# Performance work log

Hardware: AMD Instinct MI355X
Metric: run time of the kernel (lower is better)

Reference implementation:

```python
import jax, jax.numpy as jnp
import numpy as np

B, T, N, E = 4, 16, 1024, 16384
F_IN, H, FF, NH, L, C = 128, 256, 1024, 8, 2, 10
HD = H // NH
EPS = 1e-5


def setup_inputs() -> dict:
    key = jax.random.key(0)
    ks = jax.random.split(key, 12)
    g = lambda k, s: jax.random.normal(k, s, dtype=jnp.float32) * 0.02
    return {
        "x": jax.random.normal(ks[0], (B, T, N, F_IN), dtype=jnp.float32),
        "edge_index": jax.random.randint(ks[1], (B, T, 2, E), 0, N, dtype=jnp.int32),
        # GraphSAGE layer 1 (PyG SAGEConv: lin_l on mean-aggregated neighbors, lin_r on self)
        "sage1_Wl": g(ks[2], (F_IN, H)), "sage1_bl": jnp.zeros((H,), jnp.float32),
        "sage1_Wr": g(ks[3], (F_IN, H)),
        # GraphSAGE layer 2
        "sage2_Wl": g(ks[4], (H, H)), "sage2_bl": jnp.zeros((H,), jnp.float32),
        "sage2_Wr": g(ks[5], (H, H)),
        # TransformerEncoder, stacked over L layers
        "Wqkv": g(ks[6], (L, H, 3 * H)), "bqkv": jnp.zeros((L, 3 * H), jnp.float32),
        "Wo": g(ks[7], (L, H, H)), "bo": jnp.zeros((L, H), jnp.float32),
        "ln1_s": jnp.ones((L, H), jnp.float32), "ln1_b": jnp.zeros((L, H), jnp.float32),
        "W1": g(ks[8], (L, H, FF)), "b1": jnp.zeros((L, FF), jnp.float32),
        "W2": g(ks[9], (L, FF, H)), "b2": jnp.zeros((L, H), jnp.float32),
        "ln2_s": jnp.ones((L, H), jnp.float32), "ln2_b": jnp.zeros((L, H), jnp.float32),
        # final classifier
        "fc_W": g(ks[10], (H, C)), "fc_b": jnp.zeros((C,), jnp.float32),
    }


def _sage_conv(x, src, dst, Wl, bl, Wr):
    # mean neighbor aggregation: for each target node, mean of source features
    deg = jax.ops.segment_sum(jnp.ones((E,), x.dtype), dst, num_segments=N)
    agg = jax.ops.segment_sum(x[src], dst, num_segments=N)  # [N, F]
    agg = agg / jnp.clip(deg, 1.0)[:, None]
    return agg @ Wl + bl + x @ Wr


def _layernorm(x, s, b):
    m = jnp.mean(x, axis=-1, keepdims=True)
    v = jnp.var(x, axis=-1, keepdims=True)
    return (x - m) * jax.lax.rsqrt(v + EPS) * s + b


def _encoder_layer(h, Wqkv, bqkv, Wo, bo, ln1_s, ln1_b, W1, b1, W2, b2, ln2_s, ln2_b):
    # h: [B, T, H] -- post-norm (PyTorch default norm_first=False), relu FFN
    qkv = h @ Wqkv + bqkv  # [B, T, 3H]
    q, k, v = jnp.split(qkv, 3, axis=-1)
    sp = lambda t: t.reshape(B, T, NH, HD).transpose(0, 2, 1, 3)  # [B, NH, T, HD]
    q, k, v = sp(q), sp(k), sp(v)
    scores = jnp.einsum("bhqd,bhkd->bhqk", q, k) / np.sqrt(HD).astype(np.float32)
    attn = jax.nn.softmax(scores, axis=-1)
    ctx = jnp.einsum("bhqk,bhkd->bhqd", attn, v)
    ctx = ctx.transpose(0, 2, 1, 3).reshape(B, T, H)
    h = _layernorm(h + ctx @ Wo + bo, ln1_s, ln1_b)
    ffn = jax.nn.relu(h @ W1 + b1) @ W2 + b2
    return _layernorm(h + ffn, ln2_s, ln2_b)


def reference(x, edge_index, sage1_Wl, sage1_bl, sage1_Wr, sage2_Wl, sage2_bl,
              sage2_Wr, Wqkv, bqkv, Wo, bo, ln1_s, ln1_b, W1, b1, W2, b2,
              ln2_s, ln2_b, fc_W, fc_b):
    xf = x.reshape(B * T, N, F_IN)
    ef = edge_index.reshape(B * T, 2, E)

    def per_graph(xg, eg):
        src, dst = eg[0], eg[1]
        h = jax.nn.relu(_sage_conv(xg, src, dst, sage1_Wl, sage1_bl, sage1_Wr))
        h = _sage_conv(h, src, dst, sage2_Wl, sage2_bl, sage2_Wr)
        return jnp.mean(h, axis=0)  # mean-pool over nodes -> [H]

    emb = jax.vmap(per_graph)(xf, ef).reshape(B, T, H)

    h = emb
    for l in range(L):
        h = _encoder_layer(h, Wqkv[l], bqkv[l], Wo[l], bo[l], ln1_s[l], ln1_b[l],
                           W1[l], b1[l], W2[l], b2[l], ln2_s[l], ln2_b[l])
    return h[:, -1, :] @ fc_W + fc_b  # [B, C]
```

## Files before the change

kernel.cpp:

```cpp
#include <hip/hip_runtime.h>
#include <hip/hip_bf16.h>

#define Bc 4
#define Tc 16
#define Nc 1024
#define Ec 16384
#define FIN 128
#define Hc 256
#define FFc 1024
#define NHc 8
#define Lc 2
#define HDc 32
#define Gc 64
#define EPSc 1e-5f

typedef __bf16 v8bf __attribute__((ext_vector_type(8)));
typedef float v4f __attribute__((ext_vector_type(4)));

__global__ __launch_bounds__(1024) void prep_kernel(
        const int* __restrict__ ei, const float* __restrict__ Wl, const float* __restrict__ Wr,
        float* __restrict__ invdeg, float* __restrict__ cw, int* __restrict__ off,
        unsigned short* __restrict__ elist, float* __restrict__ uv,
        __bf16* __restrict__ pH, __bf16* __restrict__ pL) {
    __shared__ int degs[Nc];
    __shared__ float inv[Nc];
    __shared__ float cl[Nc];
    __shared__ int wsum[16];
    if (blockIdx.x >= 64) {
        int id = (blockIdx.x - 64) * 1024 + threadIdx.x;
        int t = id & 511;
        int bidOld = id >> 9;
        int lane = t >> 3, j = t & 7;
        int kc = bidOld >> 4, nt = bidOld & 15;
        int k = kc * 32 + ((lane >> 4) << 3) + j;
        int n = nt * 16 + (lane & 15);
        float wv = (k < 128) ? Wl[(size_t)k * Hc + n] : Wr[(size_t)(k - 128) * Hc + n];
        __bf16 hi = (__bf16)wv;
        pH[id] = hi;
        pL[id] = (__bf16)(wv - (float)hi);
        return;
    }
    int g = blockIdx.x, t = threadIdx.x;
    const int* src = ei + (size_t)g * 2 * Ec;
    const int* dst = src + Ec;
    if (t < 512) uv[g * 512 + t] = 0.f;
    degs[t] = 0; cl[t] = 0.f;
    __syncthreads();
    for (int e = t; e < Ec; e += 1024) atomicAdd(&degs[dst[e] & (Nc - 1)], 1);
    __syncthreads();
    float iv = 1.0f / fmaxf((float)degs[t], 1.0f);
    inv[t] = iv;
    invdeg[g * Nc + t] = iv;
    __syncthreads();
    for (int e = t; e < Ec; e += 1024) atomicAdd(&cl[src[e] & (Nc - 1)], inv[dst[e] & (Nc - 1)]);
    __syncthreads();
    cw[g * Nc + t] = cl[t];
    int own = degs[t];
    int lane = t & 63, wv2 = t >> 6;
    int val = own;
#pragma unroll
    for (int ofs = 1; ofs < 64; ofs <<= 1) {
        int v = __shfl_up(val, ofs, 64);
        if (lane >= ofs) val += v;
    }
    if (lane == 63) wsum[wv2] = val;
    __syncthreads();
    if (wv2 == 0 && lane < 16) {
        int wval = wsum[lane];
#pragma unroll
        for (int ofs = 1; ofs < 16; ofs <<= 1) {
            int v = __shfl_up(wval, ofs, 64);
            if (lane >= ofs) wval += v;
        }
        wsum[lane] = wval;
    }
    __syncthreads();
    int incl = val + ((wv2 > 0) ? wsum[wv2 - 1] : 0);
    int excl = incl - own;
    off[g * 1032 + t] = excl;
    if (t == 1023) off[g * 1032 + Nc] = incl;
    degs[t] = excl;
    __syncthreads();
    for (int e = t; e < Ec; e += 1024) {
        int d = dst[e] & (Nc - 1);
        int slot = atomicAdd(&degs[d], 1);
        elist[(size_t)g * Ec + slot] = (unsigned short)(src[e] & (Nc - 1));
    }
}

__global__ __launch_bounds__(512, 4) void sage_kernel(
        const float* __restrict__ x, const unsigned short* __restrict__ elist,
        const int* __restrict__ off, const float* __restrict__ invdeg,
        const float* __restrict__ cw, const __bf16* __restrict__ pH,
        const __bf16* __restrict__ pL, const float* __restrict__ bias,
        float* __restrict__ uv) {
    __shared__ __bf16 AH[64 * 264];
    __shared__ __bf16 AL[64 * 264];
    int tid = threadIdx.x, bid = blockIdx.x;
    int g = bid & 63, cc = bid >> 6, r0 = cc * 64;
    const unsigned short* el = elist + (size_t)g * Ec;
    const float* xg = x + (size_t)g * Nc * FIN;

    {
        int lr = tid >> 3, ch = tid & 7;
        int n = r0 + lr;
        int o0 = off[g * 1032 + n], o1 = off[g * 1032 + n + 1];
        float4 a0 = {0.f,0.f,0.f,0.f}, a1 = a0, a2 = a0, a3 = a0;
        const float* xc = xg + ch * 16;
        int e = o0;
        for (; e + 4 <= o1; e += 4) {
            int s0 = el[e], s1 = el[e+1], s2 = el[e+2], s3 = el[e+3];
            const float4* p0 = (const float4*)(xc + (size_t)s0 * FIN);
            const float4* p1 = (const float4*)(xc + (size_t)s1 * FIN);
            const float4* p2 = (const float4*)(xc + (size_t)s2 * FIN);
            const float4* p3 = (const float4*)(xc + (size_t)s3 * FIN);
            float4 v00=p0[0], v01=p0[1], v02=p0[2], v03=p0[3];
            float4 v10=p1[0], v11=p1[1], v12=p1[2], v13=p1[3];
            float4 v20=p2[0], v21=p2[1], v22=p2[2], v23=p2[3];
            float4 v30=p3[0], v31=p3[1], v32=p3[2], v33=p3[3];
            a0.x += v00.x+v10.x+v20.x+v30.x; a0.y += v00.y+v10.y+v20.y+v30.y;
            a0.z += v00.z+v10.z+v20.z+v30.z; a0.w += v00.w+v10.w+v20.w+v30.w;
            a1.x += v01.x+v11.x+v21.x+v31.x; a1.y += v01.y+v11.y+v21.y+v31.y;
            a1.z += v01.z+v11.z+v21.z+v31.z; a1.w += v01.w+v11.w+v21.w+v31.w;
            a2.x += v02.x+v12.x+v22.x+v32.x; a2.y += v02.y+v12.y+v22.y+v32.y;
            a2.z += v02.z+v12.z+v22.z+v32.z; a2.w += v02.w+v12.w+v22.w+v32.w;
            a3.x += v03.x+v13.x+v23.x+v33.x; a3.y += v03.y+v13.y+v23.y+v33.y;
            a3.z += v03.z+v13.z+v23.z+v33.z; a3.w += v03.w+v13.w+v23.w+v33.w;
        }
        for (; e < o1; ++e) {
            const float4* p = (const float4*)(xc + (size_t)el[e] * FIN);
            float4 v0=p[0], v1=p[1], v2=p[2], v3=p[3];
            a0.x+=v0.x; a0.y+=v0.y; a0.z+=v0.z; a0.w+=v0.w;
            a1.x+=v1.x; a1.y+=v1.y; a1.z+=v1.z; a1.w+=v1.w;
            a2.x+=v2.x; a2.y+=v2.y; a2.z+=v2.z; a2.w+=v2.w;
            a3.x+=v3.x; a3.y+=v3.y; a3.z+=v3.z; a3.w+=v3.w;
        }
        float iv = invdeg[g * Nc + n];
        float vals[16] = {a0.x*iv,a0.y*iv,a0.z*iv,a0.w*iv, a1.x*iv,a1.y*iv,a1.z*iv,a1.w*iv,
                          a2.x*iv,a2.y*iv,a2.z*iv,a2.w*iv, a3.x*iv,a3.y*iv,a3.z*iv,a3.w*iv};
        v8bf h0, h1v, l0, l1v;
#pragma unroll
        for (int i = 0; i < 8; ++i) {
            __bf16 hb = (__bf16)vals[i];
            h0[i] = hb; l0[i] = (__bf16)(vals[i] - (float)hb);
            __bf16 hb2 = (__bf16)vals[i+8];
            h1v[i] = hb2; l1v[i] = (__bf16)(vals[i+8] - (float)hb2);
        }
        __bf16* dh = &AH[lr * 264 + ch * 16];
        __bf16* dl = &AL[lr * 264 + ch * 16];
        *(v8bf*)dh = h0; *(v8bf*)(dh + 8) = h1v;
        *(v8bf*)dl = l0; *(v8bf*)(dl + 8) = l1v;
        const float4* xr = (const float4*)(xg + (size_t)n * FIN + ch * 16);
        float4 x0 = xr[0], x1 = xr[1], x2 = xr[2], x3 = xr[3];
        float xv[16] = {x0.x,x0.y,x0.z,x0.w, x1.x,x1.y,x1.z,x1.w,
                        x2.x,x2.y,x2.z,x2.w, x3.x,x3.y,x3.z,x3.w};
#pragma unroll
        for (int i = 0; i < 8; ++i) {
            __bf16 hb = (__bf16)xv[i];
            h0[i] = hb; l0[i] = (__bf16)(xv[i] - (float)hb);
            __bf16 hb2 = (__bf16)xv[i+8];
            h1v[i] = hb2; l1v[i] = (__bf16)(xv[i+8] - (float)hb2);
        }
        dh = &AH[lr * 264 + 128 + ch * 16];
        dl = &AL[lr * 264 + 128 + ch * 16];
        *(v8bf*)dh = h0; *(v8bf*)(dh + 8) = h1v;
        *(v8bf*)dl = l0; *(v8bf*)(dl + 8) = l1v;
    }
    __syncthreads();

    int w = tid >> 6, lane = tid & 63, quad = lane >> 4, lm = lane & 15;
    v4f acc[4][2];
#pragma unroll
    for (int m = 0; m < 4; ++m) { acc[m][0] = (v4f)0.f; acc[m][1] = (v4f)0.f; }
    const v8bf* wpH = (const v8bf*)pH;
    const v8bf* wpL = (const v8bf*)pL;
    for (int kc = 0; kc < 8; ++kc) {
        v8bf bH0 = wpH[(kc * 16 + 2 * w    ) * 64 + lane];
        v8bf bL0 = wpL[(kc * 16 + 2 * w    ) * 64 + lane];
        v8bf bH1 = wpH[(kc * 16 + 2 * w + 1) * 64 + lane];
        v8bf bL1 = wpL[(kc * 16 + 2 * w + 1) * 64 + lane];
#pragma unroll
        for (int mt = 0; mt < 4; ++mt) {
            int ao = (mt * 16 + lm) * 264 + kc * 32 + quad * 8;
            v8bf aH = *(const v8bf*)&AH[ao];
            v8bf aL = *(const v8bf*)&AL[ao];
            acc[mt][0] = __builtin_amdgcn_mfma_f32_16x16x32_bf16(aH, bH0, acc[mt][0], 0, 0, 0);
            acc[mt][0] = __builtin_amdgcn_mfma_f32_16x16x32_bf16(aL, bH0, acc[mt][0], 0, 0, 0);
            acc[mt][0] = __builtin_amdgcn_mfma_f32_16x16x32_bf16(aH, bL0, acc[mt][0], 0, 0, 0);
            acc[mt][1] = __builtin_amdgcn_mfma_f32_16x16x32_bf16(aH, bH1, acc[mt][1], 0, 0, 0);
            acc[mt][1] = __builtin_amdgcn_mfma_f32_16x16x32_bf16(aL, bH1, acc[mt][1], 0, 0, 0);
            acc[mt][1] = __builtin_amdgcn_mfma_f32_16x16x32_bf16(aH, bL1, acc[mt][1], 0, 0, 0);
        }
    }
#pragma unroll
    for (int j = 0; j < 2; ++j) {
        int col = (2 * w + j) * 16 + lm;
        float bcol = bias[col];
        float su = 0.f, sv = 0.f;
#pragma unroll
        for (int mt = 0; mt < 4; ++mt) {
            int nb = g * Nc + r0 + mt * 16 + quad * 4;
#pragma unroll
            for (int r = 0; r < 4; ++r) {
                float val = fmaxf(acc[mt][j][r] + bcol, 0.f);
                sv += val;
                su += cw[nb + r] * val;
            }
        }
        su += __shfl_xor(su, 16); sv += __shfl_xor(sv, 16);
        su += __shfl_xor(su, 32); sv += __shfl_xor(sv, 32);
        if (quad == 0) {
            atomicAdd(&uv[g * 512 + col], su);
            atomicAdd(&uv[g * 512 + 256 + col], sv);
        }
    }
}

__device__ __forceinline__ void gemm16(
        const float* __restrict__ A, int As,
        const float* __restrict__ W, int N, int K,
        const float* __restrict__ bias,
        float* __restrict__ O, int Os, int relu, int accum, int tid) {
    int w = tid >> 6, lane = tid & 63, quad = lane >> 4, lm = lane & 15;
    int ntot = N >> 4, kcs = K >> 5;
    for (int nt = w; nt < ntot; nt += 16) {
        v4f acc = (v4f)0.f;
        for (int kc = 0; kc < kcs; ++kc) {
            const float* ap = A + lm * As + kc * 32 + quad * 8;
            float4 f0 = *(const float4*)ap;
            float4 f1 = *(const float4*)(ap + 4);
            float av[8] = {f0.x, f0.y, f0.z, f0.w, f1.x, f1.y, f1.z, f1.w};
            v8bf aH, aL, bH, bL;
            const float* wp = W + (size_t)(kc * 32 + quad * 8) * N + nt * 16 + lm;
#pragma unroll
            for (int j = 0; j < 8; ++j) {
                __bf16 ah = (__bf16)av[j];
                aH[j] = ah; aL[j] = (__bf16)(av[j] - (float)ah);
                float wv = wp[(size_t)j * N];
                __bf16 wh = (__bf16)wv;
                bH[j] = wh; bL[j] = (__bf16)(wv - (float)wh);
            }
            acc = __builtin_amdgcn_mfma_f32_16x16x32_bf16(aH, bH, acc, 0, 0, 0);
            acc = __builtin_amdgcn_mfma_f32_16x16x32_bf16(aL, bH, acc, 0, 0, 0);
            acc = __builtin_amdgcn_mfma_f32_16x16x32_bf16(aH, bL, acc, 0, 0, 0);
        }
        int col = nt * 16 + lm;
        float bv = bias ? bias[col] : 0.f;
#pragma unroll
        for (int r = 0; r < 4; ++r) {
            int tok = quad * 4 + r;
            float val = acc[r] + bv;
            if (relu) val = fmaxf(val, 0.f);
            if (accum) O[tok * Os + col] += val;
            else       O[tok * Os + col] = val;
        }
    }
}

__device__ __forceinline__ void ln16(const float* __restrict__ pre, const float* __restrict__ res,
                                     const float* __restrict__ sc_, const float* __restrict__ bi,
                                     float* __restrict__ out, int tid) {
    int w = tid >> 6, lane = tid & 63;
    float4 pv = *(const float4*)&pre[w * 260 + lane * 4];
    float4 rv = *(const float4*)&res[w * 260 + lane * 4];
    float x0 = pv.x + rv.x, x1 = pv.y + rv.y, x2 = pv.z + rv.z, x3 = pv.w + rv.w;
    float s = x0 + x1 + x2 + x3;
    float q = x0*x0 + x1*x1 + x2*x2 + x3*x3;
#pragma unroll
    for (int o = 1; o < 64; o <<= 1) { s += __shfl_xor(s, o); q += __shfl_xor(q, o); }
    float m = s * (1.0f / 256.0f);
    float var = q * (1.0f / 256.0f) - m * m;
    float rstd = rsqrtf(var + EPSc);
    float4 sv = *(const float4*)&sc_[lane * 4];
    float4 bv = *(const float4*)&bi[lane * 4];
    float4 ov;
    ov.x = (x0 - m) * rstd * sv.x + bv.x;
    ov.y = (x1 - m) * rstd * sv.y + bv.y;
    ov.z = (x2 - m) * rstd * sv.z + bv.z;
    ov.w = (x3 - m) * rstd * sv.w + bv.w;
    *(float4*)&out[w * 260 + lane * 4] = ov;
}

__global__ __launch_bounds__(1024) void mega_kernel(
        const float* __restrict__ uv,
        const float* __restrict__ Wl2, const float* __restrict__ bl2, const float* __restrict__ Wr2,
        const float* __restrict__ Wqkv, const float* __restrict__ bqkv,
        const float* __restrict__ Wo, const float* __restrict__ bo,
        const float* __restrict__ ln1s, const float* __restrict__ ln1b,
        const float* __restrict__ W1, const float* __restrict__ b1,
        const float* __restrict__ W2, const float* __restrict__ b2,
        const float* __restrict__ ln2s, const float* __restrict__ ln2b,
        const float* __restrict__ fcW, const float* __restrict__ fcb,
        float* __restrict__ out) {
    __shared__ float h[16 * 260];
    __shared__ float big[16 * 1028];
    __shared__ float ctx[16 * 260];
    __shared__ float pre[16 * 260];
    __shared__ float h1[16 * 260];
    __shared__ float sc[2048];
    int b = blockIdx.x, tid = threadIdx.x;

    for (int i = tid; i < 16 * 512; i += 1024) {
        int tok = i >> 9, k = i & 511;
        big[tok * 516 + k] = uv[(size_t)(b * 16 + tok) * 512 + k] * (1.0f / 1024.0f);
    }
    __syncthreads();
    gemm16(big,       516, Wl2, 256, 256, bl2,     h, 260, 0, 0, tid);
    __syncthreads();
    gemm16(big + 256, 516, Wr2, 256, 256, nullptr, h, 260, 0, 1, tid);
    __syncthreads();

    for (int l = 0; l < Lc; ++l) {
        gemm16(h, 260, Wqkv + (size_t)l * Hc * 768, 768, 256, bqkv + l * 768, big, 772, 0, 0, tid);
        __syncthreads();
#pragma unroll
        for (int rep = 0; rep < 2; ++rep) {
            int idx = rep * 1024 + tid;
            int hd = idx >> 8, qt = (idx >> 4) & 15, kt = idx & 15;
            float s = 0.f;
#pragma unroll
            for (int d = 0; d < 32; ++d)
                s += big[qt * 772 + hd * 32 + d] * big[kt * 772 + 256 + hd * 32 + d];
            sc[idx] = s * 0.17677669529663687f;
        }
        __syncthreads();
        if (tid < 128) {
            int base = tid * 16;
            float m = sc[base];
            for (int j = 1; j < 16; ++j) m = fmaxf(m, sc[base + j]);
            float ev[16], sum = 0.f;
            for (int j = 0; j < 16; ++j) { ev[j] = expf(sc[base + j] - m); sum += ev[j]; }
            float inv = 1.0f / sum;
            for (int j = 0; j < 16; ++j) sc[base + j] = ev[j] * inv;
        }
        __syncthreads();
#pragma unroll
        for (int rep = 0; rep < 4; ++rep) {
            int idx = rep * 1024 + tid;
            int qt = idx >> 8, c = idx & 255;
            int hd = c >> 5, d = c & 31;
            float o = 0.f;
#pragma unroll
            for (int j = 0; j < 16; ++j)
                o += sc[hd * 256 + qt * 16 + j] * big[j * 772 + 512 + hd * 32 + d];
            ctx[qt * 260 + c] = o;
        }
        __syncthreads();
        gemm16(ctx, 260, Wo + (size_t)l * 65536, 256, 256, bo + l * 256, pre, 260, 0, 0, tid);
        __syncthreads();
        ln16(pre, h, ln1s + l * 256, ln1b + l * 256, h1, tid);
        __syncthreads();
        gemm16(h1, 260, W1 + (size_t)l * 262144, 1024, 256, b1 + l * 1024, big, 1028, 1, 0, tid);
        __syncthreads();
        gemm16(big, 1028, W2 + (size_t)l * 262144, 256, 1024, b2 + l * 256, pre, 260, 0, 0, tid);
        __syncthreads();
        ln16(pre, h1, ln2s + l * 256, ln2b + l * 256, h, tid);
        __syncthreads();
    }
    if (tid < 10) {
        float v = fcb[tid];
        for (int k = 0; k < 256; ++k) v += h[15 * 260 + k] * fcW[(size_t)k * 10 + tid];
        out[b * 10 + tid] = v;
    }
}

extern "C" void kernel_launch(void* const* d_in, const int* in_sizes, int n_in,
                              void* d_out, int out_size, void* d_ws, size_t ws_size,
                              hipStream_t stream) {
    (void)in_sizes; (void)n_in; (void)out_size; (void)ws_size;
    const float* x    = (const float*)d_in[0];
    const int*   ei   = (const int*)d_in[1];
    const float* s1Wl = (const float*)d_in[2];
    const float* s1bl = (const float*)d_in[3];
    const float* s1Wr = (const float*)d_in[4];
    const float* s2Wl = (const float*)d_in[5];
    const float* s2bl = (const float*)d_in[6];
    const float* s2Wr = (const float*)d_in[7];
    const float* Wqkv = (const float*)d_in[8];
    const float* bqkv = (const float*)d_in[9];
    const float* Wo   = (const float*)d_in[10];
    const float* bo   = (const float*)d_in[11];
    const float* ln1s = (const float*)d_in[12];
    const float* ln1b = (const float*)d_in[13];
    const float* W1   = (const float*)d_in[14];
    const float* b1   = (const float*)d_in[15];
    const float* W2   = (const float*)d_in[16];
    const float* b2   = (const float*)d_in[17];
    const float* ln2s = (const float*)d_in[18];
    const float* ln2b = (const float*)d_in[19];
    const float* fcW  = (const float*)d_in[20];
    const float* fcb  = (const float*)d_in[21];

    char* ws = (char*)d_ws;
    __bf16*         pH     = (__bf16*)(ws + 0);
    __bf16*         pL     = (__bf16*)(ws + 131072);
    float*          invdeg = (float*)(ws + 262144);
    float*          cw     = (float*)(ws + 524288);
    int*            off    = (int*)(ws + 786432);
    unsigned short* elist  = (unsigned short*)(ws + 1050624);
    float*          uv     = (float*)(ws + 3147776);

    prep_kernel<<<128, 1024, 0, stream>>>(ei, s1Wl, s1Wr, invdeg, cw, off, elist, uv, pH, pL);
    sage_kernel<<<Gc * 16, 512, 0, stream>>>(x, elist, off, invdeg, cw, pH, pL, s1bl, uv);
    mega_kernel<<<Bc, 1024, 0, stream>>>(uv, s2Wl, s2bl, s2Wr, Wqkv, bqkv, Wo, bo,
                                         ln1s, ln1b, W1, b1, W2, b2, ln2s, ln2b,
                                         fcW, fcb, (float*)d_out);
}
```

Before: 355.7 us.

## Split transformer across 64 blocks with grid barriers and prepacked bf16 weights

Replaces the 4-block mega kernel with a 64-block transformer kernel: each batch uses 16 cooperating blocks that share column tiles of every GEMM and synchronise through global atomic barriers. All transformer and SAGE-2 weights are prepacked into hi/lo bf16 MFMA layouts in the prep kernel, so the per-iteration fp32-to-bf16 split of weights goes away. The activation low-part MFMA is dropped in both the SAGE and transformer GEMMs, and SAGE occupancy is raised by removing the AL buffer. This trades accuracy for fewer MFMAs and adds spin-barrier overhead plus global round-trips for intermediates.

```diff
diff --git a/kernel.cpp b/kernel.cpp
--- a/kernel.cpp
+++ b/kernel.cpp
@@ -13,34 +13,69 @@
 #define HDc 32
 #define Gc 64
 #define EPSc 1e-5f
+#define TPACK 1703936
 
 typedef __bf16 v8bf __attribute__((ext_vector_type(8)));
+typedef __bf16 v4bf __attribute__((ext_vector_type(4)));
 typedef float v4f __attribute__((ext_vector_type(4)));
 
 __global__ __launch_bounds__(1024) void prep_kernel(
-        const int* __restrict__ ei, const float* __restrict__ Wl, const float* __restrict__ Wr,
+        const int* __restrict__ ei,
+        const float* __restrict__ Wl, const float* __restrict__ Wr,
+        const float* __restrict__ Wl2, const float* __restrict__ Wr2,
+        const float* __restrict__ Wqkv, const float* __restrict__ Wo,
+        const float* __restrict__ W1, const float* __restrict__ W2,
         float* __restrict__ invdeg, float* __restrict__ cw, int* __restrict__ off,
         unsigned short* __restrict__ elist, float* __restrict__ uv,
-        __bf16* __restrict__ pH, __bf16* __restrict__ pL) {
+        __bf16* __restrict__ sgH, __bf16* __restrict__ sgL,
+        __bf16* __restrict__ PT, int* __restrict__ bars) {
     __shared__ int degs[Nc];
     __shared__ float inv[Nc];
     __shared__ float cl[Nc];
     __shared__ int wsum[16];
+    int t = threadIdx.x;
+    if (blockIdx.x >= 128) {
+        size_t base = (size_t)(blockIdx.x - 128) * 1024 + t;
+        for (size_t idx = base; idx < TPACK; idx += 262144) {
+            size_t local; int NT, N; const float* src;
+            if (idx < 131072)       { local = idx;           NT = 16; N = 256;  src = nullptr; }
+            else if (idx < 327680)  { local = idx - 131072;  NT = 48; N = 768;  src = Wqkv; }
+            else if (idx < 524288)  { local = idx - 327680;  NT = 48; N = 768;  src = Wqkv + 196608; }
+            else if (idx < 589824)  { local = idx - 524288;  NT = 16; N = 256;  src = Wo; }
+            else if (idx < 655360)  { local = idx - 589824;  NT = 16; N = 256;  src = Wo + 65536; }
+            else if (idx < 917504)  { local = idx - 655360;  NT = 64; N = 1024; src = W1; }
+            else if (idx < 1179648) { local = idx - 917504;  NT = 64; N = 1024; src = W1 + 262144; }
+            else if (idx < 1441792) { local = idx - 1179648; NT = 16; N = 256;  src = W2; }
+            else                    { local = idx - 1441792; NT = 16; N = 256;  src = W2 + 262144; }
+            int j = local & 7, lane = (local >> 3) & 63;
+            int t2 = (int)(local >> 9);
+            int nt = t2 % NT, kc = t2 / NT;
+            int k = kc * 32 + ((lane >> 4) << 3) + j;
+            int n = nt * 16 + (lane & 15);
+            float v;
+            if (src) v = src[(size_t)k * N + n];
+            else v = (k < 256) ? Wl2[(size_t)k * 256 + n] : Wr2[(size_t)(k - 256) * 256 + n];
+            __bf16 hi = (__bf16)v;
+            PT[idx] = hi;
+            PT[TPACK + idx] = (__bf16)(v - (float)hi);
+        }
+        return;
+    }
     if (blockIdx.x >= 64) {
-        int id = (blockIdx.x - 64) * 1024 + threadIdx.x;
-        int t = id & 511;
-        int bidOld = id >> 9;
-        int lane = t >> 3, j = t & 7;
+        int id = (blockIdx.x - 64) * 1024 + t;
+        int tt = id & 511, bidOld = id >> 9;
+        int lane = tt >> 3, j = tt & 7;
         int kc = bidOld >> 4, nt = bidOld & 15;
         int k = kc * 32 + ((lane >> 4) << 3) + j;
         int n = nt * 16 + (lane & 15);
         float wv = (k < 128) ? Wl[(size_t)k * Hc + n] : Wr[(size_t)(k - 128) * Hc + n];
         __bf16 hi = (__bf16)wv;
-        pH[id] = hi;
-        pL[id] = (__bf16)(wv - (float)hi);
+        sgH[id] = hi;
+        sgL[id] = (__bf16)(wv - (float)hi);
         return;
     }
-    int g = blockIdx.x, t = threadIdx.x;
+    int g = blockIdx.x;
+    if (g == 0 && t < 16) bars[t] = 0;
     const int* src = ei + (size_t)g * 2 * Ec;
     const int* dst = src + Ec;
     if (t < 512) uv[g * 512 + t] = 0.f;
@@ -88,83 +123,57 @@
     }
 }
 
-__global__ __launch_bounds__(512, 4) void sage_kernel(
+__global__ __launch_bounds__(512, 8) void sage_kernel(
         const float* __restrict__ x, const unsigned short* __restrict__ elist,
         const int* __restrict__ off, const float* __restrict__ invdeg,
-        const float* __restrict__ cw, const __bf16* __restrict__ pH,
-        const __bf16* __restrict__ pL, const float* __restrict__ bias,
+        const float* __restrict__ cw, const __bf16* __restrict__ sgH,
+        const __bf16* __restrict__ sgL, const float* __restrict__ bias,
         float* __restrict__ uv) {
     __shared__ __bf16 AH[64 * 264];
-    __shared__ __bf16 AL[64 * 264];
     int tid = threadIdx.x, bid = blockIdx.x;
     int g = bid & 63, cc = bid >> 6, r0 = cc * 64;
     const unsigned short* el = elist + (size_t)g * Ec;
     const float* xg = x + (size_t)g * Nc * FIN;
 
-    {
-        int lr = tid >> 3, ch = tid & 7;
+    for (int it = tid; it < 1024; it += 512) {
+        int lr = it >> 4, ch = it & 15;
         int n = r0 + lr;
         int o0 = off[g * 1032 + n], o1 = off[g * 1032 + n + 1];
-        float4 a0 = {0.f,0.f,0.f,0.f}, a1 = a0, a2 = a0, a3 = a0;
-        const float* xc = xg + ch * 16;
+        float4 a0 = {0.f, 0.f, 0.f, 0.f}, a1 = a0;
+        const float* xc = xg + ch * 8;
         int e = o0;
         for (; e + 4 <= o1; e += 4) {
-            int s0 = el[e], s1 = el[e+1], s2 = el[e+2], s3 = el[e+3];
+            int s0 = el[e], s1 = el[e + 1], s2 = el[e + 2], s3 = el[e + 3];
             const float4* p0 = (const float4*)(xc + (size_t)s0 * FIN);
             const float4* p1 = (const float4*)(xc + (size_t)s1 * FIN);
             const float4* p2 = (const float4*)(xc + (size_t)s2 * FIN);
             const float4* p3 = (const float4*)(xc + (size_t)s3 * FIN);
-            float4 v00=p0[0], v01=p0[1], v02=p0[2], v03=p0[3];
-            float4 v10=p1[0], v11=p1[1], v12=p1[2], v13=p1[3];
-            float4 v20=p2[0], v21=p2[1], v22=p2[2], v23=p2[3];
-            float4 v30=p3[0], v31=p3[1], v32=p3[2], v33=p3[3];
-            a0.x += v00.x+v10.x+v20.x+v30.x; a0.y += v00.y+v10.y+v20.y+v30.y;
-            a0.z += v00.z+v10.z+v20.z+v30.z; a0.w += v00.w+v10.w+v20.w+v30.w;
-            a1.x += v01.x+v11.x+v21.x+v31.x; a1.y += v01.y+v11.y+v21.y+v31.y;
-            a1.z += v01.z+v11.z+v21.z+v31.z; a1.w += v01.w+v11.w+v21.w+v31.w;
-            a2.x += v02.x+v12.x+v22.x+v32.x; a2.y += v02.y+v12.y+v22.y+v32.y;
-            a2.z += v02.z+v12.z+v22.z+v32.z; a2.w += v02.w+v12.w+v22.w+v32.w;
-            a3.x += v03.x+v13.x+v23.x+v33.x; a3.y += v03.y+v13.y+v23.y+v33.y;
-            a3.z += v03.z+v13.z+v23.z+v33.z; a3.w += v03.w+v13.w+v23.w+v33.w;
+            float4 u0 = p0[0], v0 = p0[1], u1 = p1[0], v1 = p1[1];
+            float4 u2 = p2[0], v2 = p2[1], u3 = p3[0], v3 = p3[1];
+            a0.x += u0.x + u1.x + u2.x + u3.x; a0.y += u0.y + u1.y + u2.y + u3.y;
+            a0.z += u0.z + u1.z + u2.z + u3.z; a0.w += u0.w + u1.w + u2.w + u3.w;
+            a1.x += v0.x + v1.x + v2.x + v3.x; a1.y += v0.y + v1.y + v2.y + v3.y;
+            a1.z += v0.z + v1.z + v2.z + v3.z; a1.w += v0.w + v1.w + v2.w + v3.w;
         }
         for (; e < o1; ++e) {
             const float4* p = (const float4*)(xc + (size_t)el[e] * FIN);
-            float4 v0=p[0], v1=p[1], v2=p[2], v3=p[3];
-            a0.x+=v0.x; a0.y+=v0.y; a0.z+=v0.z; a0.w+=v0.w;
-            a1.x+=v1.x; a1.y+=v1.y; a1.z+=v1.z; a1.w+=v1.w;
-            a2.x+=v2.x; a2.y+=v2.y; a2.z+=v2.z; a2.w+=v2.w;
-            a3.x+=v3.x; a3.y+=v3.y; a3.z+=v3.z; a3.w+=v3.w;
+            float4 u0 = p[0], v0 = p[1];
+            a0.x += u0.x; a0.y += u0.y; a0.z += u0.z; a0.w += u0.w;
+            a1.x += v0.x; a1.y += v0.y; a1.z += v0.z; a1.w += v0.w;
         }
         float iv = invdeg[g * Nc + n];
-        float vals[16] = {a0.x*iv,a0.y*iv,a0.z*iv,a0.w*iv, a1.x*iv,a1.y*iv,a1.z*iv,a1.w*iv,
-                          a2.x*iv,a2.y*iv,a2.z*iv,a2.w*iv, a3.x*iv,a3.y*iv,a3.z*iv,a3.w*iv};
-        v8bf h0, h1v, l0, l1v;
-#pragma unroll
-        for (int i = 0; i < 8; ++i) {
-            __bf16 hb = (__bf16)vals[i];
-            h0[i] = hb; l0[i] = (__bf16)(vals[i] - (float)hb);
-            __bf16 hb2 = (__bf16)vals[i+8];
-            h1v[i] = hb2; l1v[i] = (__bf16)(vals[i+8] - (float)hb2);
-        }
-        __bf16* dh = &AH[lr * 264 + ch * 16];
-        __bf16* dl = &AL[lr * 264 + ch * 16];
-        *(v8bf*)dh = h0; *(v8bf*)(dh + 8) = h1v;
-        *(v8bf*)dl = l0; *(v8bf*)(dl + 8) = l1v;
-        const float4* xr = (const float4*)(xg + (size_t)n * FIN + ch * 16);
-        float4 x0 = xr[0], x1 = xr[1], x2 = xr[2], x3 = xr[3];
-        float xv[16] = {x0.x,x0.y,x0.z,x0.w, x1.x,x1.y,x1.z,x1.w,
-                        x2.x,x2.y,x2.z,x2.w, x3.x,x3.y,x3.z,x3.w};
-#pragma unroll
-        for (int i = 0; i < 8; ++i) {
-            __bf16 hb = (__bf16)xv[i];
-            h0[i] = hb; l0[i] = (__bf16)(xv[i] - (float)hb);
-            __bf16 hb2 = (__bf16)xv[i+8];
-            h1v[i] = hb2; l1v[i] = (__bf16)(xv[i+8] - (float)hb2);
-        }
-        dh = &AH[lr * 264 + 128 + ch * 16];
-        dl = &AL[lr * 264 + 128 + ch * 16];
-        *(v8bf*)dh = h0; *(v8bf*)(dh + 8) = h1v;
-        *(v8bf*)dl = l0; *(v8bf*)(dl + 8) = l1v;
+        v8bf oa;
+        oa[0] = (__bf16)(a0.x * iv); oa[1] = (__bf16)(a0.y * iv);
+        oa[2] = (__bf16)(a0.z * iv); oa[3] = (__bf16)(a0.w * iv);
+        oa[4] = (__bf16)(a1.x * iv); oa[5] = (__bf16)(a1.y * iv);
+        oa[6] = (__bf16)(a1.z * iv); oa[7] = (__bf16)(a1.w * iv);
+        *(v8bf*)&AH[lr * 264 + ch * 8] = oa;
+        const float4* xr = (const float4*)(xg + (size_t)n * FIN + ch * 8);
+        float4 x0 = xr[0], x1 = xr[1];
+        v8bf ox;
+        ox[0] = (__bf16)x0.x; ox[1] = (__bf16)x0.y; ox[2] = (__bf16)x0.z; ox[3] = (__bf16)x0.w;
+        ox[4] = (__bf16)x1.x; ox[5] = (__bf16)x1.y; ox[6] = (__bf16)x1.z; ox[7] = (__bf16)x1.w;
+        *(v8bf*)&AH[lr * 264 + 128 + ch * 8] = ox;
     }
     __syncthreads();
 
@@ -172,8 +181,8 @@
     v4f acc[4][2];
 #pragma unroll
     for (int m = 0; m < 4; ++m) { acc[m][0] = (v4f)0.f; acc[m][1] = (v4f)0.f; }
-    const v8bf* wpH = (const v8bf*)pH;
-    const v8bf* wpL = (const v8bf*)pL;
+    const v8bf* wpH = (const v8bf*)sgH;
+    const v8bf* wpL = (const v8bf*)sgL;
     for (int kc = 0; kc < 8; ++kc) {
         v8bf bH0 = wpH[(kc * 16 + 2 * w    ) * 64 + lane];
         v8bf bL0 = wpL[(kc * 16 + 2 * w    ) * 64 + lane];
@@ -181,14 +190,10 @@
         v8bf bL1 = wpL[(kc * 16 + 2 * w + 1) * 64 + lane];
 #pragma unroll
         for (int mt = 0; mt < 4; ++mt) {
-            int ao = (mt * 16 + lm) * 264 + kc * 32 + quad * 8;
-            v8bf aH = *(const v8bf*)&AH[ao];
-            v8bf aL = *(const v8bf*)&AL[ao];
+            v8bf aH = *(const v8bf*)&AH[(mt * 16 + lm) * 264 + kc * 32 + quad * 8];
             acc[mt][0] = __builtin_amdgcn_mfma_f32_16x16x32_bf16(aH, bH0, acc[mt][0], 0, 0, 0);
-            acc[mt][0] = __builtin_amdgcn_mfma_f32_16x16x32_bf16(aL, bH0, acc[mt][0], 0, 0, 0);
             acc[mt][0] = __builtin_amdgcn_mfma_f32_16x16x32_bf16(aH, bL0, acc[mt][0], 0, 0, 0);
             acc[mt][1] = __builtin_amdgcn_mfma_f32_16x16x32_bf16(aH, bH1, acc[mt][1], 0, 0, 0);
-            acc[mt][1] = __builtin_amdgcn_mfma_f32_16x16x32_bf16(aL, bH1, acc[mt][1], 0, 0, 0);
             acc[mt][1] = __builtin_amdgcn_mfma_f32_16x16x32_bf16(aH, bL1, acc[mt][1], 0, 0, 0);
         }
     }
@@ -216,151 +221,228 @@
     }
 }
 
-__device__ __forceinline__ void gemm16(
-        const float* __restrict__ A, int As,
-        const float* __restrict__ W, int N, int K,
-        const float* __restrict__ bias,
-        float* __restrict__ O, int Os, int relu, int accum, int tid) {
+__device__ __forceinline__ void gbar(int* cnt, int* gen, int nb) {
+    __syncthreads();
+    if (threadIdx.x == 0) {
+        __threadfence();
+        int g = __hip_atomic_load(gen, __ATOMIC_RELAXED, __HIP_MEMORY_SCOPE_AGENT);
+        int prev = __hip_atomic_fetch_add(cnt, 1, __ATOMIC_ACQ_REL, __HIP_MEMORY_SCOPE_AGENT);
+        if (prev == nb - 1) {
+            __hip_atomic_store(cnt, 0, __ATOMIC_RELAXED, __HIP_MEMORY_SCOPE_AGENT);
+            __hip_atomic_fetch_add(gen, 1, __ATOMIC_RELEASE, __HIP_MEMORY_SCOPE_AGENT);
+        } else {
+            while (__hip_atomic_load(gen, __ATOMIC_ACQUIRE, __HIP_MEMORY_SCOPE_AGENT) == g)
+                __builtin_amdgcn_s_sleep(4);
+        }
+        __threadfence();
+    }
+    __syncthreads();
+}
+
+__device__ __forceinline__ v4f mfma_nt(const __bf16* AH, int As, const __bf16* PT,
+                                       int segOff, int NT, int nt, int kcs, int lane) {
+    int quad = lane >> 4, lm = lane & 15;
+    v4f acc = (v4f)0.f;
+    const __bf16* BH = PT + segOff;
+    const __bf16* BL = PT + TPACK + segOff;
+    for (int kc = 0; kc < kcs; ++kc) {
+        v8bf a = *(const v8bf*)(AH + lm * As + kc * 32 + quad * 8);
+        size_t bo_ = ((size_t)(kc * NT + nt) * 64 + lane) * 8;
+        v8bf bH = *(const v8bf*)(BH + bo_);
+        v8bf bL = *(const v8bf*)(BL + bo_);
+        acc = __builtin_amdgcn_mfma_f32_16x16x32_bf16(a, bH, acc, 0, 0, 0);
+        acc = __builtin_amdgcn_mfma_f32_16x16x32_bf16(a, bL, acc, 0, 0, 0);
+    }
+    return acc;
+}
+
+__device__ __forceinline__ void stage_AH(const float* src, int g0, int K, int srcStride,
+                                         float scale, __bf16* AH, int As, int tid) {
+    int Kq = K >> 2;
+    for (int i = tid; i < 16 * Kq; i += 256) {
+        int row = i / Kq, c = i - row * Kq;
+        float4 v = *(const float4*)(src + (size_t)(g0 + row) * srcStride + c * 4);
+        v4bf o;
+        o[0] = (__bf16)(v.x * scale); o[1] = (__bf16)(v.y * scale);
+        o[2] = (__bf16)(v.z * scale); o[3] = (__bf16)(v.w * scale);
+        *(v4bf*)(AH + row * As + c * 4) = o;
+    }
+}
+
+__device__ __forceinline__ void ln_stage(const float* src, int g0, const float* s,
+                                         const float* bln, __bf16* AH, float* hout, int tid) {
+    int w = tid >> 6, lane = tid & 63;
+    for (int t = w; t < 16; t += 4) {
+        const float* row = src + (size_t)(g0 + t) * 256;
+        float4 v = *(const float4*)(row + lane * 4);
+        float sm = v.x + v.y + v.z + v.w;
+        float sq = v.x * v.x + v.y * v.y + v.z * v.z + v.w * v.w;
+#pragma unroll
+        for (int o = 1; o < 64; o <<= 1) { sm += __shfl_xor(sm, o); sq += __shfl_xor(sq, o); }
+        float m = sm * (1.0f / 256.0f);
+        float var = sq * (1.0f / 256.0f) - m * m;
+        float rs = rsqrtf(var + EPSc);
+        float4 sv = *(const float4*)(s + lane * 4);
+        float4 bv = *(const float4*)(bln + lane * 4);
+        float o0 = (v.x - m) * rs * sv.x + bv.x, o1 = (v.y - m) * rs * sv.y + bv.y;
+        float o2 = (v.z - m) * rs * sv.z + bv.z, o3 = (v.w - m) * rs * sv.w + bv.w;
+        v4bf ob;
+        ob[0] = (__bf16)o0; ob[1] = (__bf16)o1; ob[2] = (__bf16)o2; ob[3] = (__bf16)o3;
+        *(v4bf*)(AH + t * 264 + lane * 4) = ob;
+        if (hout) {
+            float4 ov = {o0, o1, o2, o3};
+            *(float4*)(hout + (size_t)(g0 + t) * 256 + lane * 4) = ov;
+        }
+    }
+}
+
+__global__ __launch_bounds__(256) void xform_kernel(
+        const float* __restrict__ uv, const __bf16* __restrict__ PT,
+        const float* __restrict__ bl2, const float* __restrict__ bqkv,
+        const float* __restrict__ bo, const float* __restrict__ ln1s,
+        const float* __restrict__ ln1b, const float* __restrict__ b1f,
+        const float* __restrict__ b2f, const float* __restrict__ ln2s,
+        const float* __restrict__ ln2b, const float* __restrict__ fcW,
+        const float* __restrict__ fcb,
+        float* __restrict__ h, float* __restrict__ qkvg, float* __restrict__ h1,
+        float* __restrict__ pre2, float* __restrict__ f,
+        int* __restrict__ bars, float* __restrict__ out) {
+    __shared__ __align__(16) char smem[66560];
+    int tid = threadIdx.x;
+    int b = blockIdx.x >> 4, sb = blockIdx.x & 15;
     int w = tid >> 6, lane = tid & 63, quad = lane >> 4, lm = lane & 15;
-    int ntot = N >> 4, kcs = K >> 5;
-    for (int nt = w; nt < ntot; nt += 16) {
-        v4f acc = (v4f)0.f;
-        for (int kc = 0; kc < kcs; ++kc) {
-            const float* ap = A + lm * As + kc * 32 + quad * 8;
-            float4 f0 = *(const float4*)ap;
-            float4 f1 = *(const float4*)(ap + 4);
-            float av[8] = {f0.x, f0.y, f0.z, f0.w, f1.x, f1.y, f1.z, f1.w};
-            v8bf aH, aL, bH, bL;
-            const float* wp = W + (size_t)(kc * 32 + quad * 8) * N + nt * 16 + lm;
-#pragma unroll
-            for (int j = 0; j < 8; ++j) {
-                __bf16 ah = (__bf16)av[j];
-                aH[j] = ah; aL[j] = (__bf16)(av[j] - (float)ah);
-                float wv = wp[(size_t)j * N];
-                __bf16 wh = (__bf16)wv;
-                bH[j] = wh; bL[j] = (__bf16)(wv - (float)wh);
-            }
-            acc = __builtin_amdgcn_mfma_f32_16x16x32_bf16(aH, bH, acc, 0, 0, 0);
-            acc = __builtin_amdgcn_mfma_f32_16x16x32_bf16(aL, bH, acc, 0, 0, 0);
-            acc = __builtin_amdgcn_mfma_f32_16x16x32_bf16(aH, bL, acc, 0, 0, 0);
-        }
-        int col = nt * 16 + lm;
-        float bv = bias ? bias[col] : 0.f;
-#pragma unroll
-        for (int r = 0; r < 4; ++r) {
-            int tok = quad * 4 + r;
-            float val = acc[r] + bv;
-            if (relu) val = fmaxf(val, 0.f);
-            if (accum) O[tok * Os + col] += val;
-            else       O[tok * Os + col] = val;
-        }
-    }
-}
-
-__device__ __forceinline__ void ln16(const float* __restrict__ pre, const float* __restrict__ res,
-                                     const float* __restrict__ sc_, const float* __restrict__ bi,
-                                     float* __restrict__ out, int tid) {
-    int w = tid >> 6, lane = tid & 63;
-    float4 pv = *(const float4*)&pre[w * 260 + lane * 4];
-    float4 rv = *(const float4*)&res[w * 260 + lane * 4];
-    float x0 = pv.x + rv.x, x1 = pv.y + rv.y, x2 = pv.z + rv.z, x3 = pv.w + rv.w;
-    float s = x0 + x1 + x2 + x3;
-    float q = x0*x0 + x1*x1 + x2*x2 + x3*x3;
-#pragma unroll
-    for (int o = 1; o < 64; o <<= 1) { s += __shfl_xor(s, o); q += __shfl_xor(q, o); }
-    float m = s * (1.0f / 256.0f);
-    float var = q * (1.0f / 256.0f) - m * m;
-    float rstd = rsqrtf(var + EPSc);
-    float4 sv = *(const float4*)&sc_[lane * 4];
-    float4 bv = *(const float4*)&bi[lane * 4];
-    float4 ov;
-    ov.x = (x0 - m) * rstd * sv.x + bv.x;
-    ov.y = (x1 - m) * rstd * sv.y + bv.y;
-    ov.z = (x2 - m) * rstd * sv.z + bv.z;
-    ov.w = (x3 - m) * rstd * sv.w + bv.w;
-    *(float4*)&out[w * 260 + lane * 4] = ov;
-}
-
-__global__ __launch_bounds__(1024) void mega_kernel(
-        const float* __restrict__ uv,
-        const float* __restrict__ Wl2, const float* __restrict__ bl2, const float* __restrict__ Wr2,
-        const float* __restrict__ Wqkv, const float* __restrict__ bqkv,
-        const float* __restrict__ Wo, const float* __restrict__ bo,
-        const float* __restrict__ ln1s, const float* __restrict__ ln1b,
-        const float* __restrict__ W1, const float* __restrict__ b1,
-        const float* __restrict__ W2, const float* __restrict__ b2,
-        const float* __restrict__ ln2s, const float* __restrict__ ln2b,
-        const float* __restrict__ fcW, const float* __restrict__ fcb,
-        float* __restrict__ out) {
-    __shared__ float h[16 * 260];
-    __shared__ float big[16 * 1028];
-    __shared__ float ctx[16 * 260];
-    __shared__ float pre[16 * 260];
-    __shared__ float h1[16 * 260];
-    __shared__ float sc[2048];
-    int b = blockIdx.x, tid = threadIdx.x;
-
-    for (int i = tid; i < 16 * 512; i += 1024) {
-        int tok = i >> 9, k = i & 511;
-        big[tok * 516 + k] = uv[(size_t)(b * 16 + tok) * 512 + k] * (1.0f / 1024.0f);
-    }
-    __syncthreads();
-    gemm16(big,       516, Wl2, 256, 256, bl2,     h, 260, 0, 0, tid);
-    __syncthreads();
-    gemm16(big + 256, 516, Wr2, 256, 256, nullptr, h, 260, 0, 1, tid);
-    __syncthreads();
+    int* cnt = bars + b;
+    int* gen = bars + 8 + b;
+    int g0 = b * 16;
+    __bf16* AH = (__bf16*)smem;
+
+    stage_AH(uv, g0, 512, 512, 1.0f / 1024.0f, AH, 520, tid);
+    __syncthreads();
+    if (w == 0) {
+        v4f acc = mfma_nt(AH, 520, PT, 0, 16, sb, 16, lane);
+        int col = sb * 16 + lm;
+#pragma unroll
+        for (int r = 0; r < 4; ++r)
+            h[(size_t)(g0 + quad * 4 + r) * 256 + col] = acc[r] + bl2[col];
+    }
+    gbar(cnt, gen, 16);
 
     for (int l = 0; l < Lc; ++l) {
-        gemm16(h, 260, Wqkv + (size_t)l * Hc * 768, 768, 256, bqkv + l * 768, big, 772, 0, 0, tid);
+        if (l == 0) stage_AH(h, g0, 256, 256, 1.0f, AH, 264, tid);
+        else ln_stage(pre2, g0, ln2s + (l - 1) * 256, ln2b + (l - 1) * 256, AH,
+                      (sb == 0) ? h : nullptr, tid);
         __syncthreads();
-#pragma unroll
-        for (int rep = 0; rep < 2; ++rep) {
-            int idx = rep * 1024 + tid;
-            int hd = idx >> 8, qt = (idx >> 4) & 15, kt = idx & 15;
-            float s = 0.f;
-#pragma unroll
-            for (int d = 0; d < 32; ++d)
-                s += big[qt * 772 + hd * 32 + d] * big[kt * 772 + 256 + hd * 32 + d];
-            sc[idx] = s * 0.17677669529663687f;
-        }
+        if (w < 3) {
+            int nt = sb * 3 + w;
+            v4f acc = mfma_nt(AH, 264, PT, 131072 + l * 196608, 48, nt, 8, lane);
+            int col = nt * 16 + lm;
+#pragma unroll
+            for (int r = 0; r < 4; ++r)
+                qkvg[(size_t)(g0 + quad * 4 + r) * 768 + col] = acc[r] + bqkv[l * 768 + col];
+        }
+        gbar(cnt, gen, 16);
+        {
+            float* qkvL = (float*)smem;
+            float* sc = (float*)(smem + 49408);
+            __bf16* cAH = (__bf16*)(smem + 57600);
+            for (int i = tid; i < 3072; i += 256) {
+                int row = i / 192, c = i - row * 192;
+                *(float4*)&qkvL[row * 772 + c * 4] =
+                    *(const float4*)&qkvg[(size_t)(g0 + row) * 768 + c * 4];
+            }
+            __syncthreads();
+#pragma unroll
+            for (int hd = 0; hd < 8; ++hd) {
+                int qt = tid >> 4, kt = tid & 15;
+                float s = 0.f;
+#pragma unroll
+                for (int d = 0; d < 32; ++d)
+                    s += qkvL[qt * 772 + hd * 32 + d] * qkvL[kt * 772 + 256 + hd * 32 + d];
+                sc[hd * 256 + qt * 16 + kt] = s * 0.17677669529663687f;
+            }
+            __syncthreads();
+            if (tid < 128) {
+                int base = tid * 16;
+                float m = sc[base];
+                for (int j = 1; j < 16; ++j) m = fmaxf(m, sc[base + j]);
+                float ev[16], sum = 0.f;
+                for (int j = 0; j < 16; ++j) { ev[j] = expf(sc[base + j] - m); sum += ev[j]; }
+                float inv = 1.0f / sum;
+                for (int j = 0; j < 16; ++j) sc[base + j] = ev[j] * inv;
+            }
+            __syncthreads();
+            for (int i = tid; i < 4096; i += 256) {
+                int qt = i >> 8, c = i & 255, hd = c >> 5, d = c & 31;
+                float o = 0.f;
+#pragma unroll
+                for (int j = 0; j < 16; ++j)
+                    o += sc[hd * 256 + qt * 16 + j] * qkvL[j * 772 + 512 + hd * 32 + d];
+                cAH[qt * 264 + c] = (__bf16)o;
+            }
+            __syncthreads();
+            if (w == 0) {
+                v4f acc = mfma_nt(cAH, 264, PT, 524288 + l * 65536, 16, sb, 8, lane);
+                int col = sb * 16 + lm;
+#pragma unroll
+                for (int r = 0; r < 4; ++r) {
+                    int gg = g0 + quad * 4 + r;
+                    pre2[(size_t)gg * 256 + col] =
+                        h[(size_t)gg * 256 + col] + bo[l * 256 + col] + acc[r];
+                }
+            }
+        }
+        gbar(cnt, gen, 16);
+        ln_stage(pre2, g0, ln1s + l * 256, ln1b + l * 256, AH, (sb == 0) ? h1 : nullptr, tid);
         __syncthreads();
-        if (tid < 128) {
-            int base = tid * 16;
-            float m = sc[base];
-            for (int j = 1; j < 16; ++j) m = fmaxf(m, sc[base + j]);
-            float ev[16], sum = 0.f;
-            for (int j = 0; j < 16; ++j) { ev[j] = expf(sc[base + j] - m); sum += ev[j]; }
-            float inv = 1.0f / sum;
-            for (int j = 0; j < 16; ++j) sc[base + j] = ev[j] * inv;
-        }
+        {
+            int nt = sb * 4 + w;
+            v4f acc = mfma_nt(AH, 264, PT, 655360 + l * 262144, 64, nt, 8, lane);
+            int col = nt * 16 + lm;
+#pragma unroll
+            for (int r = 0; r < 4; ++r)
+                f[(size_t)(g0 + quad * 4 + r) * 1024 + col] =
+                    fmaxf(acc[r] + b1f[l * 1024 + col], 0.f);
+        }
+        gbar(cnt, gen, 16);
+        stage_AH(f, g0, 1024, 1024, 1.0f, AH, 1032, tid);
         __syncthreads();
-#pragma unroll
-        for (int rep = 0; rep < 4; ++rep) {
-            int idx = rep * 1024 + tid;
-            int qt = idx >> 8, c = idx & 255;
-            int hd = c >> 5, d = c & 31;
-            float o = 0.f;
-#pragma unroll
-            for (int j = 0; j < 16; ++j)
-                o += sc[hd * 256 + qt * 16 + j] * big[j * 772 + 512 + hd * 32 + d];
-            ctx[qt * 260 + c] = o;
+        if (w == 0) {
+            v4f acc = mfma_nt(AH, 1032, PT, 1179648 + l * 262144, 16, sb, 32, lane);
+            int col = sb * 16 + lm;
+#pragma unroll
+            for (int r = 0; r < 4; ++r) {
+                int gg = g0 + quad * 4 + r;
+                pre2[(size_t)gg * 256 + col] =
+                    h1[(size_t)gg * 256 + col] + b2f[l * 256 + col] + acc[r];
+            }
+        }
+        gbar(cnt, gen, 16);
+    }
+    if (sb == 0) {
+        float* hrow = (float*)smem;
+        float* mrs = (float*)(smem + 1088);
+        int gg = g0 + 15;
+        if (w == 0) {
+            float4 v = *(const float4*)&pre2[(size_t)gg * 256 + lane * 4];
+            float sm = v.x + v.y + v.z + v.w;
+            float sq = v.x * v.x + v.y * v.y + v.z * v.z + v.w * v.w;
+#pragma unroll
+            for (int o = 1; o < 64; o <<= 1) { sm += __shfl_xor(sm, o); sq += __shfl_xor(sq, o); }
+            if (lane == 0) {
+                float m = sm * (1.0f / 256.0f);
+                mrs[0] = m;
+                mrs[1] = rsqrtf(sq * (1.0f / 256.0f) - m * m + EPSc);
+            }
         }
         __syncthreads();
-        gemm16(ctx, 260, Wo + (size_t)l * 65536, 256, 256, bo + l * 256, pre, 260, 0, 0, tid);
+        float m = mrs[0], rs = mrs[1];
+        hrow[tid] = (pre2[(size_t)gg * 256 + tid] - m) * rs * ln2s[256 + tid] + ln2b[256 + tid];
         __syncthreads();
-        ln16(pre, h, ln1s + l * 256, ln1b + l * 256, h1, tid);
-        __syncthreads();
-        gemm16(h1, 260, W1 + (size_t)l * 262144, 1024, 256, b1 + l * 1024, big, 1028, 1, 0, tid);
-        __syncthreads();
-        gemm16(big, 1028, W2 + (size_t)l * 262144, 256, 1024, b2 + l * 256, pre, 260, 0, 0, tid);
-        __syncthreads();
-        ln16(pre, h1, ln2s + l * 256, ln2b + l * 256, h, tid);
-        __syncthreads();
-    }
-    if (tid < 10) {
-        float v = fcb[tid];
-        for (int k = 0; k < 256; ++k) v += h[15 * 260 + k] * fcW[(size_t)k * 10 + tid];
-        out[b * 10 + tid] = v;
+        if (tid < 10) {
+            float v = fcb[tid];
+            for (int k = 0; k < 256; ++k) v += hrow[k] * fcW[(size_t)k * 10 + tid];
+            out[b * 10 + tid] = v;
+        }
     }
 }
 
@@ -392,17 +474,25 @@
     const float* fcb  = (const float*)d_in[21];
 
     char* ws = (char*)d_ws;
-    __bf16*         pH     = (__bf16*)(ws + 0);
-    __bf16*         pL     = (__bf16*)(ws + 131072);
-    float*          invdeg = (float*)(ws + 262144);
-    float*          cw     = (float*)(ws + 524288);
-    int*            off    = (int*)(ws + 786432);
-    unsigned short* elist  = (unsigned short*)(ws + 1050624);
-    float*          uv     = (float*)(ws + 3147776);
-
-    prep_kernel<<<128, 1024, 0, stream>>>(ei, s1Wl, s1Wr, invdeg, cw, off, elist, uv, pH, pL);
-    sage_kernel<<<Gc * 16, 512, 0, stream>>>(x, elist, off, invdeg, cw, pH, pL, s1bl, uv);
-    mega_kernel<<<Bc, 1024, 0, stream>>>(uv, s2Wl, s2bl, s2Wr, Wqkv, bqkv, Wo, bo,
-                                         ln1s, ln1b, W1, b1, W2, b2, ln2s, ln2b,
-                                         fcW, fcb, (float*)d_out);
-}
+    __bf16*         PT     = (__bf16*)(ws + 0);
+    __bf16*         sgH    = (__bf16*)(ws + 6815744);
+    __bf16*         sgL    = (__bf16*)(ws + 6946816);
+    float*          invdeg = (float*)(ws + 7077888);
+    float*          cw     = (float*)(ws + 7340032);
+    int*            off    = (int*)(ws + 7602176);
+    unsigned short* elist  = (unsigned short*)(ws + 7866368);
+    float*          uv     = (float*)(ws + 9963520);
+    float*          h      = (float*)(ws + 10094592);
+    float*          qkvg   = (float*)(ws + 10160128);
+    float*          h1     = (float*)(ws + 10356736);
+    float*          pre2   = (float*)(ws + 10422272);
+    float*          f      = (float*)(ws + 10487808);
+    int*            bars   = (int*)(ws + 10749952);
+
+    prep_kernel<<<384, 1024, 0, stream>>>(ei, s1Wl, s1Wr, s2Wl, s2Wr, Wqkv, Wo, W1, W2,
+                                          invdeg, cw, off, elist, uv, sgH, sgL, PT, bars);
+    sage_kernel<<<Gc * 16, 512, 0, stream>>>(x, elist, off, invdeg, cw, sgH, sgL, s1bl, uv);
+    xform_kernel<<<Gc, 256, 0, stream>>>(uv, PT, s2bl, bqkv, bo, ln1s, ln1b, b1, b2,
+                                         ln2s, ln2b, fcW, fcb, h, qkvg, h1, pre2, f,
+                                         bars, (float*)d_out);
+}
```

Result: faster. 341.0 us (-4.1%).
